# Performance work log

Hardware: AMD Instinct MI355X
Metric: run time of the kernel (lower is better)

## Reference

```python
import jax, jax.numpy as jnp
import numpy as np

ALPHA = 0.2  # module hardcodes a = 0.2


def _triplet_total(outputs, labels):
    # Faithful vectorization of the nested-loop mining:
    #  - sort samples by label (stable, like python sorted with key=label)
    #  - anchor p1 = first element of each contiguous label group
    #  - positives p2 = remaining members of the group; ap = ||p1-p2||^2
    #  - negatives = every sample with a different label
    #  - per (p2, neg): add (ap - an + alpha) for an in {||p1-n||^2, ||p2-n||^2}
    #    iff ap < an and ap - an + alpha > 0  (i.e. 0 < an - ap < alpha)
    order = jnp.argsort(labels)          # stable sort, matches python sorted
    x = outputs[order]                   # [n, d]
    lab = labels[order]                  # [n]
    n = x.shape[0]
    idx = jnp.arange(n)
    is_start = jnp.concatenate([jnp.ones((1,), bool), lab[1:] != lab[:-1]])
    # index of the group-start (anchor) for every position
    anchor_of = jax.lax.cummax(jnp.where(is_start, idx, 0))

    # pairwise squared distances Dm[i,j] = ||x_i - x_j||^2
    sq = jnp.sum(x * x, axis=-1)                       # [n]
    Dm = sq[:, None] + sq[None, :] - 2.0 * (x @ x.T)   # [n, n]

    ap = Dm[anchor_of, idx]   # [n]   ||p1 - p2||^2 for each potential positive
    an1 = Dm[anchor_of, :]    # [n,n] ||p1 - neg||^2
    an2 = Dm                  # [n,n] ||p2 - neg||^2

    pos_mask = ~is_start                         # p2 ranges over non-anchor rows
    neg_mask = lab[:, None] != lab[None, :]      # negatives: different label
    valid = pos_mask[:, None] & neg_mask         # [n, n]

    def hinge(an):
        d = ap[:, None] - an
        return jnp.where((d < 0) & (d + ALPHA > 0), d + ALPHA, 0.0)

    contrib = jnp.where(valid, hinge(an1) + hinge(an2), 0.0)
    return jnp.sum(contrib)


def setup_inputs() -> dict:
    key = jax.random.key(0)
    k1, k2 = jax.random.split(key)
    N, D, C = 8192, 128, 512
    outputs = jax.random.normal(k1, (N, D), dtype=jnp.float32)
    labels = jax.random.randint(k2, (N,), 0, C, dtype=jnp.int32)
    return {"outputs": outputs, "labels": labels}


def reference(outputs, labels):
    return _triplet_total(outputs, labels)
```

## Files before the change

### kernel.cpp

```cpp
#include <hip/hip_runtime.h>
#include <limits.h>
#include <stdint.h>

#define ALPHA 0.2f
#define HALFA 0.1f
static constexpr int N = 8192;
static constexpr int D = 128;
static constexpr int C = 512;
static constexpr int BT = 128;
static constexpr int GR = D / 8;
static constexpr int SL = BT + 1;
static constexpr int MAXG = 64;
static constexpr int NB = N / BT;
static constexpr int NT1 = (C / 64) * (N / BT);
static constexpr int NSP = NB / 2;
static constexpr int SPB = 16;
static constexpr int GRID = NT1 + NSP * SPB;

using half8    = __attribute__((ext_vector_type(8))) _Float16;
using floatx16 = __attribute__((ext_vector_type(16))) float;

__device__ __forceinline__ floatx16 zerov() { floatx16 v = {0.f}; return v; }

__device__ __forceinline__ half8 cvt8(float4 v0, float4 v1) {
    half8 h;
    h[0] = (_Float16)v0.x; h[1] = (_Float16)v0.y; h[2] = (_Float16)v0.z; h[3] = (_Float16)v0.w;
    h[4] = (_Float16)v1.x; h[5] = (_Float16)v1.y; h[6] = (_Float16)v1.z; h[7] = (_Float16)v1.w;
    return h;
}

__device__ __forceinline__ float ss8(float4 v0, float4 v1) {
    return v0.x*v0.x + v0.y*v0.y + v0.z*v0.z + v0.w*v0.w
         + v1.x*v1.x + v1.y*v1.y + v1.z*v1.z + v1.w*v1.w;
}

__device__ __forceinline__ void dec_sp(int k, int t, int lenA, int& br, int& bc) {
    if (t < lenA) { br = k;      bc = k + t; }
    else          { br = 63 - k; bc = 63 - k + (t - lenA); }
}


__launch_bounds__(256)
__global__ void k_prep(const float* __restrict__ x, const int* __restrict__ labels,
                       _Float16* __restrict__ xh, float* __restrict__ sq,
                       int* __restrict__ anchorg, float* __restrict__ ap,
                       float* __restrict__ out) {
    __shared__ int sAnc[C];
    const int tid = threadIdx.x;
    if (blockIdx.x == 0 && tid == 0) out[0] = 0.f;
    for (int i = tid; i < C; i += 256) sAnc[i] = INT_MAX;
    __syncthreads();
    const int4* lab4 = (const int4*)labels;
    for (int t = tid; t < N / 4; t += 256) {
        int4 lv = lab4[t];
        int base = 4 * t;
        atomicMin(&sAnc[lv.x], base);
        atomicMin(&sAnc[lv.y], base + 1);
        atomicMin(&sAnc[lv.z], base + 2);
        atomicMin(&sAnc[lv.w], base + 3);
    }
    __syncthreads();
    if (tid < 2) {
        int c = blockIdx.x * 2 + tid;
        int a = sAnc[c];
        anchorg[c] = (a == INT_MAX) ? -1 : a;
    }

    const int r = blockIdx.x * 32 + (tid >> 3);
    const int sub = tid & 7;
    const float4* src = (const float4*)(x + (size_t)r * D) + sub * 4;
    half8* dst = (half8*)(xh + (size_t)r * D) + sub * 2;
    half8 hj[2];
    float ssj = 0.f;
#pragma unroll
    for (int i = 0; i < 2; ++i) {
        float4 v0 = src[2 * i], v1 = src[2 * i + 1];
        hj[i] = cvt8(v0, v1);
        dst[i] = hj[i];
        ssj += ss8(v0, v1);
    }
    ssj += __shfl_xor(ssj, 1); ssj += __shfl_xor(ssj, 2); ssj += __shfl_xor(ssj, 4);

    const int a = sAnc[labels[r]];
    const float4* asrc = (const float4*)(x + (size_t)a * D) + sub * 4;
    float ssa = 0.f, dot = 0.f;
#pragma unroll
    for (int i = 0; i < 2; ++i) {
        float4 a0 = asrc[2 * i], a1 = asrc[2 * i + 1];
        half8 ha = cvt8(a0, a1);
        ssa += ss8(a0, a1);
#pragma unroll
        for (int e = 0; e < 8; ++e) dot = fmaf((float)ha[e], (float)hj[i][e], dot);
    }
    ssa += __shfl_xor(ssa, 1); ssa += __shfl_xor(ssa, 2); ssa += __shfl_xor(ssa, 4);
    dot += __shfl_xor(dot, 1); dot += __shfl_xor(dot, 2); dot += __shfl_xor(dot, 4);
    if (sub == 0) {
        sq[r] = ssj;
        ap[r] = ssa + ssj - 2.f * dot;
    }
}


__launch_bounds__(512, 2)
__global__ void k_main(const _Float16* __restrict__ xh, const int* __restrict__ labels,
                       const int* __restrict__ anchor, const float* __restrict__ sq,
                       const float* __restrict__ ap, float* __restrict__ out) {
    __shared__ __align__(16) _Float16 BsH[GR * SL * 8];
    __shared__ __align__(16) float sge[64 * MAXG];
    __shared__ float4 rowE[BT];
    __shared__ float4 colE[2][BT];
    __shared__ int   sArow[64];
    __shared__ float sSqA[64];
    __shared__ int   sCnt[64];
    __shared__ float wsum[8];
    half8* Bs = (half8*)BsH;

    const int tid = threadIdx.x;
    const int lane = tid & 63, w = tid >> 6;
    const int m = lane & 31, q = lane >> 5;
    const int sg = tid & 15, sr0 = tid >> 4;
    float local = 0.f;

    if ((int)blockIdx.x < NT1) {
        const int cb = blockIdx.x >> 6, jb = blockIdx.x & 63;
        const int c0 = cb * 64, j0 = jb * BT;
        const int wr2 = w >> 2, wc4 = w & 3;

        if (tid < 64) {
            int a = anchor[c0 + tid];
            int ar = (a < 0) ? 0 : a;
            sArow[tid] = ar; sSqA[tid] = sq[ar]; sCnt[tid] = 0;
        } else if (tid < 192) {
            int j = j0 + tid - 64;
            colE[0][tid - 64] = make_float4(sq[j], __int_as_float(labels[j]), 0.f, 0.f);
        }
        {
            float4 big = make_float4(1e30f, 1e30f, 1e30f, 1e30f);
            ((float4*)sge)[tid * 2] = big; ((float4*)sge)[tid * 2 + 1] = big;
        }
        __syncthreads();

        half8 af[8];
        {
            int arow = sArow[wr2 * 32 + m];
            const half8* aptr = (const half8*)(xh + (size_t)arow * D) + q;
#pragma unroll
            for (int k = 0; k < 8; ++k) af[k] = aptr[2 * k];
        }
#pragma unroll
        for (int i = 0; i < 4; ++i) {
            int row = sr0 + 32 * i;
            Bs[sg * SL + row] = *((const half8*)(xh + (size_t)(j0 + row) * D) + sg);
        }
        {
            const int4* lab4 = (const int4*)labels;
            for (int t = tid; t < N / 4; t += 512) {
                int4 lv = lab4[t];
                int base = 4 * t;
#pragma unroll
                for (int kk = 0; kk < 4; ++kk) {
                    int l = (kk == 0) ? lv.x : (kk == 1) ? lv.y : (kk == 2) ? lv.z : lv.w;
                    int li = l - c0;
                    if ((unsigned)li < 64u) {
                        int idx = base + kk;
                        if (idx != sArow[li]) {
                            int slot = atomicAdd(&sCnt[li], 1);
                            if (slot < MAXG) sge[li * MAXG + slot] = ap[idx] + HALFA;
                        }
                    }
                }
            }
        }
        __syncthreads();

        floatx16 acc = zerov();
#pragma unroll
        for (int k = 0; k < 8; ++k) {
            half8 b0 = Bs[(2 * k + q) * SL + wc4 * 32 + m];
            acc = __builtin_amdgcn_mfma_f32_32x32x16_f16(af[k], b0, acc, 0, 0, 0);
        }

        float4 cj = colE[0][wc4 * 32 + m];
        float sqj = cj.x; int labj = __float_as_int(cj.y);
#pragma unroll
        for (int rr = 0; rr < 16; ++rr) {
            int row = wr2 * 32 + (rr & 3) + 8 * (rr >> 2) + 4 * q;
            float Dv = fmaf(-2.f, acc[rr], sSqA[row] + sqj);
            bool vld = (labj != c0 + row);
            int n = sCnt[row]; n = (n > MAXG) ? MAXG : n;
            int nf = (n + 3) & ~3;
            for (int gb = 0; gb < nf; gb += 4) {
                float4 ev = *(const float4*)&sge[row * MAXG + gb];
                float u;
                u = ev.x - Dv; if (vld && __builtin_fabsf(u) < HALFA) local += u + HALFA;
                u = ev.y - Dv; if (vld && __builtin_fabsf(u) < HALFA) local += u + HALFA;
                u = ev.z - Dv; if (vld && __builtin_fabsf(u) < HALFA) local += u + HALFA;
                u = ev.w - Dv; if (vld && __builtin_fabsf(u) < HALFA) local += u + HALFA;
            }
        }
    } else {
        const int bi = blockIdx.x - NT1;
        const int k = bi >> 4, p = bi & 15;
        const int lenA = 64 - k;
        const int wr = w >> 1, wc = w & 1;
        int cbuf = 0, cur_br = -1;
        half8 af[8], breg[4];

        {
            int br0, bc0; dec_sp(k, p, lenA, br0, bc0);
            int j0 = bc0 * BT;
#pragma unroll
            for (int i = 0; i < 4; ++i)
                breg[i] = *((const half8*)(xh + (size_t)(j0 + sr0 + 32 * i) * D) + sg);
            if (tid < BT) {
                int j = j0 + tid;
                int lj = labels[j]; int a = anchor[lj];
                float sqj = sq[j];
                float e2 = (j == a) ? -1e30f : ap[j] + HALFA - sqj;
                colE[0][tid] = make_float4(e2, __int_as_float(lj), sqj, 0.f);
            }
        }

        for (int t = p; t < 65; t += SPB) {
            int br, bc; dec_sp(k, t, lenA, br, bc);
            const int i0 = br * BT, j0n_unused = bc;
            (void)j0n_unused;
            const bool diag = (br == bc);

            if (br != cur_br) {
                cur_br = br;
                const half8* aptr = (const half8*)(xh + (size_t)(i0 + wr * 32 + m) * D) + q;
#pragma unroll
                for (int kk = 0; kk < 8; ++kk) af[kk] = aptr[2 * kk];
                if (tid < BT) {
                    int i = i0 + tid;
                    int li = labels[i]; int a = anchor[li];
                    float sqi = sq[i];
                    float e2 = (i == a) ? -1e30f : ap[i] + HALFA - sqi;
                    rowE[tid] = make_float4(e2, __int_as_float(li), sqi, 0.f);
                }
            }

#pragma unroll
            for (int i = 0; i < 4; ++i)
                Bs[sg * SL + sr0 + 32 * i] = breg[i];
            __syncthreads();

            if (t + SPB < 65) {
                int brn, bcn; dec_sp(k, t + SPB, lenA, brn, bcn);
                int j0n = bcn * BT;
#pragma unroll
                for (int i = 0; i < 4; ++i)
                    breg[i] = *((const half8*)(xh + (size_t)(j0n + sr0 + 32 * i) * D) + sg);
                if (tid < BT) {
                    int j = j0n + tid;
                    int lj = labels[j]; int a = anchor[lj];
                    float sqj = sq[j];
                    float e2 = (j == a) ? -1e30f : ap[j] + HALFA - sqj;
                    colE[cbuf ^ 1][tid] = make_float4(e2, __int_as_float(lj), sqj, 0.f);
                }
            }

            floatx16 acc0 = zerov(), acc1 = zerov();
#pragma unroll
            for (int kk = 0; kk < 8; ++kk) {
                half8 b0 = Bs[(2 * kk + q) * SL + wc * 64 + m];
                half8 b1 = Bs[(2 * kk + q) * SL + wc * 64 + 32 + m];
                acc0 = __builtin_amdgcn_mfma_f32_32x32x16_f16(af[kk], b0, acc0, 0, 0, 0);
                acc1 = __builtin_amdgcn_mfma_f32_32x32x16_f16(af[kk], b1, acc1, 0, 0, 0);
            }

            float sqjv[2], e2j[2]; int labj[2];
            { float4 cj = colE[cbuf][wc * 64 + m];      e2j[0] = cj.x; labj[0] = __float_as_int(cj.y); sqjv[0] = cj.z; }
            { float4 cj = colE[cbuf][wc * 64 + 32 + m]; e2j[1] = cj.x; labj[1] = __float_as_int(cj.y); sqjv[1] = cj.z; }

#pragma unroll
            for (int rr = 0; rr < 16; ++rr) {
                int row = wr * 32 + (rr & 3) + 8 * (rr >> 2) + 4 * q;
                float4 re = rowE[row];
                float e2i = re.x, sqi = re.z;
                int labi = __float_as_int(re.y);
                {
                    float dot = acc0[rr];
                    if (labi != labj[0]) {
                        float u2 = fmaf(2.f, dot, e2i - sqjv[0]);
                        if (__builtin_fabsf(u2) < HALFA) local += u2 + HALFA;
                        if (!diag) {
                            float u2b = fmaf(2.f, dot, e2j[0] - sqi);
                            if (__builtin_fabsf(u2b) < HALFA) local += u2b + HALFA;
                        }
                    }
                }
                {
                    float dot = acc1[rr];
                    if (labi != labj[1]) {
                        float u2 = fmaf(2.f, dot, e2i - sqjv[1]);
                        if (__builtin_fabsf(u2) < HALFA) local += u2 + HALFA;
                        if (!diag) {
                            float u2b = fmaf(2.f, dot, e2j[1] - sqi);
                            if (__builtin_fabsf(u2b) < HALFA) local += u2b + HALFA;
                        }
                    }
                }
            }
            cbuf ^= 1;
            __syncthreads();
        }
    }

#pragma unroll
    for (int off = 32; off; off >>= 1) local += __shfl_down(local, off);
    if (lane == 0) wsum[w] = local;
    __syncthreads();
    if (tid == 0) {
        float s = 0.f;
#pragma unroll
        for (int i = 0; i < 8; ++i) s += wsum[i];
        atomicAdd(out, s);
    }
}


extern "C" void kernel_launch(void* const* d_in, const int* in_sizes, int n_in,
                              void* d_out, int out_size, void* d_ws, size_t ws_size,
                              hipStream_t stream) {
    const float* x = (const float*)d_in[0];
    const int* labels = (const int*)d_in[1];
    float* out = (float*)d_out;

    char* p = (char*)d_ws;
    int* anchor = (int*)p;        p += C * 4;
    float* sq = (float*)p;        p += N * 4;
    float* ap = (float*)p;        p += N * 4;
    p = (char*)(((uintptr_t)p + 255) & ~(uintptr_t)255);
    _Float16* xh = (_Float16*)p;

    k_prep<<<N / 32, 256, 0, stream>>>(x, labels, xh, sq, anchor, ap, out);
    k_main<<<GRID, 512, 0, stream>>>(xh, labels, anchor, sq, ap, out);
}
```

Before: 113.4 us.

## Precompute per-class positive lists in prep and restructure main kernel tiling

Builds the per-class lists of positive distances (plus half-alpha) once in the prep kernel through global atomics, instead of having every main-kernel block rescan all labels to rebuild them in shared memory. The first-phase blocks now each cover two column tiles, with the second tile loaded into registers during the first tile's compute, which halves that block count. The hinge accumulation becomes branchless: it adds a constant per element and corrects with a count term at the end. It also lowers MAXG to 48, raises the launch-bounds occupancy hint to 6, and adds two memsets, which risks overflowing class lists and register spills.

Result: slower. 134.9 us (+19.0%).

```diff
diff --git a/kernel.cpp b/kernel.cpp
--- a/kernel.cpp
+++ b/kernel.cpp
@@ -10,12 +10,12 @@
 static constexpr int BT = 128;
 static constexpr int GR = D / 8;
 static constexpr int SL = BT + 1;
-static constexpr int MAXG = 64;
+static constexpr int MAXG = 48;
 static constexpr int NB = N / BT;
-static constexpr int NT1 = (C / 64) * (N / BT);
+static constexpr int NT1B = 256;
 static constexpr int NSP = NB / 2;
 static constexpr int SPB = 16;
-static constexpr int GRID = NT1 + NSP * SPB;
+static constexpr int GRID = NT1B + NSP * SPB;
 
 using half8    = __attribute__((ext_vector_type(8))) _Float16;
 using floatx16 = __attribute__((ext_vector_type(16))) float;
@@ -44,6 +44,7 @@
 __global__ void k_prep(const float* __restrict__ x, const int* __restrict__ labels,
                        _Float16* __restrict__ xh, float* __restrict__ sq,
                        int* __restrict__ anchorg, float* __restrict__ ap,
+                       int* __restrict__ ecnt, float* __restrict__ egrid,
                        float* __restrict__ out) {
     __shared__ int sAnc[C];
     const int tid = threadIdx.x;
@@ -81,7 +82,8 @@
     }
     ssj += __shfl_xor(ssj, 1); ssj += __shfl_xor(ssj, 2); ssj += __shfl_xor(ssj, 4);
 
-    const int a = sAnc[labels[r]];
+    const int lab = labels[r];
+    const int a = sAnc[lab];
     const float4* asrc = (const float4*)(x + (size_t)a * D) + sub * 4;
     float ssa = 0.f, dot = 0.f;
 #pragma unroll
@@ -95,16 +97,22 @@
     ssa += __shfl_xor(ssa, 1); ssa += __shfl_xor(ssa, 2); ssa += __shfl_xor(ssa, 4);
     dot += __shfl_xor(dot, 1); dot += __shfl_xor(dot, 2); dot += __shfl_xor(dot, 4);
     if (sub == 0) {
+        float apv = ssa + ssj - 2.f * dot;
         sq[r] = ssj;
-        ap[r] = ssa + ssj - 2.f * dot;
-    }
-}
-
-
-__launch_bounds__(512, 2)
+        ap[r] = apv;
+        if (r != a) {
+            int slot = atomicAdd(&ecnt[lab], 1);
+            if (slot < MAXG) egrid[(size_t)lab * MAXG + slot] = apv + HALFA;
+        }
+    }
+}
+
+
+__launch_bounds__(512, 6)
 __global__ void k_main(const _Float16* __restrict__ xh, const int* __restrict__ labels,
                        const int* __restrict__ anchor, const float* __restrict__ sq,
-                       const float* __restrict__ ap, float* __restrict__ out) {
+                       const float* __restrict__ ap, const int* __restrict__ ecnt,
+                       const float* __restrict__ egrid, float* __restrict__ out) {
     __shared__ __align__(16) _Float16 BsH[GR * SL * 8];
     __shared__ __align__(16) float sge[64 * MAXG];
     __shared__ float4 rowE[BT];
@@ -120,23 +128,38 @@
     const int m = lane & 31, q = lane >> 5;
     const int sg = tid & 15, sr0 = tid >> 4;
     float local = 0.f;
-
-    if ((int)blockIdx.x < NT1) {
-        const int cb = blockIdx.x >> 6, jb = blockIdx.x & 63;
-        const int c0 = cb * 64, j0 = jb * BT;
+    int cnt = 0;
+
+    if ((int)blockIdx.x < NT1B) {
+        const int cb = blockIdx.x >> 5, jg = blockIdx.x & 31;
+        const int c0 = cb * 64;
         const int wr2 = w >> 2, wc4 = w & 3;
 
         if (tid < 64) {
-            int a = anchor[c0 + tid];
+            int c = c0 + tid;
+            int a = anchor[c];
             int ar = (a < 0) ? 0 : a;
-            sArow[tid] = ar; sSqA[tid] = sq[ar]; sCnt[tid] = 0;
-        } else if (tid < 192) {
-            int j = j0 + tid - 64;
-            colE[0][tid - 64] = make_float4(sq[j], __int_as_float(labels[j]), 0.f, 0.f);
+            sArow[tid] = ar;
+            sSqA[tid] = sq[ar];
+            int n = ecnt[c];
+            sCnt[tid] = (n > MAXG) ? MAXG : n;
         }
         {
-            float4 big = make_float4(1e30f, 1e30f, 1e30f, 1e30f);
-            ((float4*)sge)[tid * 2] = big; ((float4*)sge)[tid * 2 + 1] = big;
+            const float4* srcv = (const float4*)(egrid + (size_t)c0 * MAXG);
+            float4* dstv = (float4*)sge;
+            dstv[tid] = srcv[tid];
+            if (tid < 64 * MAXG / 4 - 512) dstv[tid + 512] = srcv[tid + 512];
+        }
+        half8 breg[4];
+        {
+            int j0 = (jg * 2) * BT;
+#pragma unroll
+            for (int i = 0; i < 4; ++i)
+                breg[i] = *((const half8*)(xh + (size_t)(j0 + sr0 + 32 * i) * D) + sg);
+            if (tid < BT) {
+                int j = j0 + tid;
+                colE[0][tid] = make_float4(sq[j], __int_as_float(labels[j]), 0.f, 0.f);
+            }
         }
         __syncthreads();
 
@@ -147,59 +170,53 @@
 #pragma unroll
             for (int k = 0; k < 8; ++k) af[k] = aptr[2 * k];
         }
-#pragma unroll
-        for (int i = 0; i < 4; ++i) {
-            int row = sr0 + 32 * i;
-            Bs[sg * SL + row] = *((const half8*)(xh + (size_t)(j0 + row) * D) + sg);
-        }
-        {
-            const int4* lab4 = (const int4*)labels;
-            for (int t = tid; t < N / 4; t += 512) {
-                int4 lv = lab4[t];
-                int base = 4 * t;
-#pragma unroll
-                for (int kk = 0; kk < 4; ++kk) {
-                    int l = (kk == 0) ? lv.x : (kk == 1) ? lv.y : (kk == 2) ? lv.z : lv.w;
-                    int li = l - c0;
-                    if ((unsigned)li < 64u) {
-                        int idx = base + kk;
-                        if (idx != sArow[li]) {
-                            int slot = atomicAdd(&sCnt[li], 1);
-                            if (slot < MAXG) sge[li * MAXG + slot] = ap[idx] + HALFA;
-                        }
-                    }
-                }
-            }
-        }
-        __syncthreads();
-
-        floatx16 acc = zerov();
-#pragma unroll
-        for (int k = 0; k < 8; ++k) {
-            half8 b0 = Bs[(2 * k + q) * SL + wc4 * 32 + m];
-            acc = __builtin_amdgcn_mfma_f32_32x32x16_f16(af[k], b0, acc, 0, 0, 0);
-        }
-
-        float4 cj = colE[0][wc4 * 32 + m];
-        float sqj = cj.x; int labj = __float_as_int(cj.y);
-#pragma unroll
-        for (int rr = 0; rr < 16; ++rr) {
-            int row = wr2 * 32 + (rr & 3) + 8 * (rr >> 2) + 4 * q;
-            float Dv = fmaf(-2.f, acc[rr], sSqA[row] + sqj);
-            bool vld = (labj != c0 + row);
-            int n = sCnt[row]; n = (n > MAXG) ? MAXG : n;
-            int nf = (n + 3) & ~3;
-            for (int gb = 0; gb < nf; gb += 4) {
-                float4 ev = *(const float4*)&sge[row * MAXG + gb];
-                float u;
-                u = ev.x - Dv; if (vld && __builtin_fabsf(u) < HALFA) local += u + HALFA;
-                u = ev.y - Dv; if (vld && __builtin_fabsf(u) < HALFA) local += u + HALFA;
-                u = ev.z - Dv; if (vld && __builtin_fabsf(u) < HALFA) local += u + HALFA;
-                u = ev.w - Dv; if (vld && __builtin_fabsf(u) < HALFA) local += u + HALFA;
-            }
+
+        for (int t = 0; t < 2; ++t) {
+#pragma unroll
+            for (int i = 0; i < 4; ++i)
+                Bs[sg * SL + sr0 + 32 * i] = breg[i];
+            __syncthreads();
+
+            if (t == 0) {
+                int j1 = (jg * 2 + 1) * BT;
+#pragma unroll
+                for (int i = 0; i < 4; ++i)
+                    breg[i] = *((const half8*)(xh + (size_t)(j1 + sr0 + 32 * i) * D) + sg);
+                if (tid < BT) {
+                    int j = j1 + tid;
+                    colE[1][tid] = make_float4(sq[j], __int_as_float(labels[j]), 0.f, 0.f);
+                }
+            }
+
+            floatx16 acc = zerov();
+#pragma unroll
+            for (int k = 0; k < 8; ++k) {
+                half8 b0 = Bs[(2 * k + q) * SL + wc4 * 32 + m];
+                acc = __builtin_amdgcn_mfma_f32_32x32x16_f16(af[k], b0, acc, 0, 0, 0);
+            }
+
+            float4 cj = colE[t][wc4 * 32 + m];
+            float sqj = cj.x; int labj = __float_as_int(cj.y);
+#pragma unroll
+            for (int rr = 0; rr < 16; ++rr) {
+                int row = wr2 * 32 + (rr & 3) + 8 * (rr >> 2) + 4 * q;
+                float Dv = fmaf(-2.f, acc[rr], sSqA[row] + sqj);
+                Dv = (labj != c0 + row) ? Dv : 3.0e38f;
+                int nf = (sCnt[row] + 3) & ~3;
+                cnt += nf;
+                for (int gb = 0; gb < nf; gb += 4) {
+                    float4 ev = *(const float4*)&sge[row * MAXG + gb];
+                    float u;
+                    u = ev.x - Dv; local += (__builtin_fabsf(u) < HALFA) ? u : -HALFA;
+                    u = ev.y - Dv; local += (__builtin_fabsf(u) < HALFA) ? u : -HALFA;
+                    u = ev.z - Dv; local += (__builtin_fabsf(u) < HALFA) ? u : -HALFA;
+                    u = ev.w - Dv; local += (__builtin_fabsf(u) < HALFA) ? u : -HALFA;
+                }
+            }
+            __syncthreads();
         }
     } else {
-        const int bi = blockIdx.x - NT1;
+        const int bi = blockIdx.x - NT1B;
         const int k = bi >> 4, p = bi & 15;
         const int lenA = 64 - k;
         const int wr = w >> 1, wc = w & 1;
@@ -223,8 +240,7 @@
 
         for (int t = p; t < 65; t += SPB) {
             int br, bc; dec_sp(k, t, lenA, br, bc);
-            const int i0 = br * BT, j0n_unused = bc;
-            (void)j0n_unused;
+            const int i0 = br * BT;
             const bool diag = (br == bc);
 
             if (br != cur_br) {
@@ -280,34 +296,27 @@
                 float4 re = rowE[row];
                 float e2i = re.x, sqi = re.z;
                 int labi = __float_as_int(re.y);
-                {
-                    float dot = acc0[rr];
-                    if (labi != labj[0]) {
-                        float u2 = fmaf(2.f, dot, e2i - sqjv[0]);
-                        if (__builtin_fabsf(u2) < HALFA) local += u2 + HALFA;
-                        if (!diag) {
-                            float u2b = fmaf(2.f, dot, e2j[0] - sqi);
-                            if (__builtin_fabsf(u2b) < HALFA) local += u2b + HALFA;
-                        }
+#pragma unroll
+                for (int tn = 0; tn < 2; ++tn) {
+                    float dot = (tn == 0) ? acc0[rr] : acc1[rr];
+                    bool ne = (labi != labj[tn]);
+                    float b1 = ne ? (e2i - sqjv[tn]) : 3.0e38f;
+                    float u2 = fmaf(2.f, dot, b1);
+                    local += (__builtin_fabsf(u2) < HALFA) ? u2 : -HALFA;
+                    if (!diag) {
+                        float b2 = ne ? (e2j[tn] - sqi) : 3.0e38f;
+                        float u2b = fmaf(2.f, dot, b2);
+                        local += (__builtin_fabsf(u2b) < HALFA) ? u2b : -HALFA;
                     }
                 }
-                {
-                    float dot = acc1[rr];
-                    if (labi != labj[1]) {
-                        float u2 = fmaf(2.f, dot, e2i - sqjv[1]);
-                        if (__builtin_fabsf(u2) < HALFA) local += u2 + HALFA;
-                        if (!diag) {
-                            float u2b = fmaf(2.f, dot, e2j[1] - sqi);
-                            if (__builtin_fabsf(u2b) < HALFA) local += u2b + HALFA;
-                        }
-                    }
-                }
-            }
+            }
+            cnt += diag ? 32 : 64;
             cbuf ^= 1;
             __syncthreads();
         }
     }
 
+    local += HALFA * (float)cnt;
 #pragma unroll
     for (int off = 32; off; off >>= 1) local += __shfl_down(local, off);
     if (lane == 0) wsum[w] = local;
@@ -332,9 +341,13 @@
     int* anchor = (int*)p;        p += C * 4;
     float* sq = (float*)p;        p += N * 4;
     float* ap = (float*)p;        p += N * 4;
+    int* ecnt = (int*)p;          p += C * 4;
+    float* egrid = (float*)p;     p += (size_t)C * MAXG * 4;
     p = (char*)(((uintptr_t)p + 255) & ~(uintptr_t)255);
     _Float16* xh = (_Float16*)p;
 
-    k_prep<<<N / 32, 256, 0, stream>>>(x, labels, xh, sq, anchor, ap, out);
-    k_main<<<GRID, 512, 0, stream>>>(xh, labels, anchor, sq, ap, out);
-}
+    hipMemsetAsync(ecnt, 0, C * 4, stream);
+    hipMemsetAsync(egrid, 0x7F, (size_t)C * MAXG * 4, stream);
+    k_prep<<<N / 32, 256, 0, stream>>>(x, labels, xh, sq, anchor, ap, ecnt, egrid, out);
+    k_main<<<GRID, 512, 0, stream>>>(xh, labels, anchor, sq, ap, ecnt, egrid, out);
+}
```
